# Kernel tuning notes

Hardware: AMD Instinct MI355X
Metric: run time of the kernel (lower is better)

Reference implementation:

```python
import jax, jax.numpy as jnp
import numpy as np

IN_CH, OUT_CH, K, DIL = 64, 128, 3, 8

def setup_inputs() -> dict:
    key = jax.random.key(0)
    k1, k2, k3 = jax.random.split(key, 3)
    x = jax.random.normal(k1, (16, IN_CH, 128, 128), dtype=jnp.float32)
    # xavier_normal-like init for W
    fan_in, fan_out = IN_CH * K * K, OUT_CH * K * K
    std = (2.0 / (fan_in + fan_out)) ** 0.5
    W = jax.random.normal(k2, (OUT_CH, IN_CH, K, K), dtype=jnp.float32) * std
    b = jax.random.normal(k3, (OUT_CH,), dtype=jnp.float32)
    return {"x": x, "W": W, "b": b}

def reference(x, W, b):
    pad = DIL * (K // 2)  # circular halo so output spatial size == input
    xp = jnp.pad(x, ((0, 0), (0, 0), (pad, pad), (pad, pad)), mode="wrap")
    y = jax.lax.conv_general_dilated(
        xp, W,
        window_strides=(1, 1),
        padding="VALID",
        rhs_dilation=(DIL, DIL),
        dimension_numbers=("NCHW", "OIHW", "NCHW"),
    )
    return y + b[None, :, None, None]
```

## Files before the change

kernel.cpp:

```cpp
#include <hip/hip_runtime.h>

#define IN_CH 64
#define OUT_CH 128
#define HW 128
#define KTAPS 9
#define ROWB 16384
#define ATILE 16384

typedef __bf16 bf16x8 __attribute__((ext_vector_type(8)));
typedef float f32x16 __attribute__((ext_vector_type(16)));
typedef float f32x4 __attribute__((ext_vector_type(4)));

__device__ __forceinline__ unsigned f2bf(float f) {
    unsigned u = __builtin_bit_cast(unsigned, f);
    return (u + 0x7FFFu + ((u >> 16) & 1u)) >> 16;
}

__device__ __forceinline__ int swz(int r) { return ((r ^ (r >> 3)) & 7) << 4; }

__device__ __forceinline__ void gload_lds16(const void* g, void* l) {
    __builtin_amdgcn_global_load_lds(
        (const __attribute__((address_space(1))) unsigned int*)g,
        (__attribute__((address_space(3))) unsigned int*)l, 16, 0, 0);
}

__global__ void wprep_kernel(const float* __restrict__ W, unsigned short* __restrict__ Wl) {
    int i = blockIdx.x * blockDim.x + threadIdx.x;
    if (i >= OUT_CH * IN_CH * KTAPS) return;
    int tap = i >> 13;
    int oc  = (i >> 6) & 127;
    int ic  = i & 63;
    int kh = tap / 3, kw = tap % 3;
    float v = W[((oc * IN_CH + ic) * 3 + kh) * 3 + kw];
    int addr = (oc * 128 + ic * 2) ^ swz(oc);
    *(unsigned short*)((unsigned char*)Wl + tap * ATILE + addr) = (unsigned short)f2bf(v);
}

__global__ __launch_bounds__(256, 2) void conv_kernel_f(
    const float* __restrict__ x, const unsigned short* __restrict__ Wl,
    const float* __restrict__ bias, float* __restrict__ y)
{
    __shared__ __align__(16) unsigned char xsB[3 * ROWB];
    __shared__ __align__(16) unsigned char xsA[2 * ATILE];

    int bid = blockIdx.x;
    int sb  = (bid & 7) * 256 + (bid >> 3);
    int n = sb >> 7, h = sb & 127;
    int tid = threadIdx.x;
    int wid = tid >> 6, lane = tid & 63;

    {
        const unsigned char* asrc = (const unsigned char*)Wl;
        #pragma unroll
        for (int j = 0; j < 4; ++j) {
            int off = wid * 4096 + j * 1024;
            gload_lds16(asrc + off + lane * 16, xsA + off);
        }
    }
    #pragma unroll
    for (int it = 0; it < 3; ++it) {
        int q   = it * 256 + tid;
        int w4  = q & 31;
        int ic8 = (q >> 5) & 7;
        int kh  = q >> 8;
        int srow = (h + kh * 8 + 120) & 127;
        const float* xp = x + (((n * IN_CH + ic8 * 8) * HW + srow) * HW + w4 * 4);
        f32x4 v[8];
        #pragma unroll
        for (int j = 0; j < 8; ++j)
            v[j] = *reinterpret_cast<const f32x4*>(xp + j * (HW * HW));
        #pragma unroll
        for (int j2 = 0; j2 < 4; ++j2) {
            int w = w4 * 4 + j2;
            uint4 pk;
            pk.x = f2bf(v[0][j2]) | (f2bf(v[1][j2]) << 16);
            pk.y = f2bf(v[2][j2]) | (f2bf(v[3][j2]) << 16);
            pk.z = f2bf(v[4][j2]) | (f2bf(v[5][j2]) << 16);
            pk.w = f2bf(v[6][j2]) | (f2bf(v[7][j2]) << 16);
            *reinterpret_cast<uint4*>(xsB + kh * ROWB + ((w * 128 + ic8 * 16) ^ swz(w))) = pk;
        }
    }
    __syncthreads();

    int wr = wid >> 1, wc = wid & 1;
    int l31 = lane & 31, lhi = lane >> 5;

    f32x16 acc[2][2];
    #pragma unroll
    for (int a = 0; a < 2; ++a)
        #pragma unroll
        for (int bq = 0; bq < 2; ++bq)
            #pragma unroll
            for (int r = 0; r < 16; ++r) acc[a][bq][r] = 0.0f;

    int arow0 = wr * 64 + l31, arow1 = arow0 + 32;
    int aoff0 = arow0 * 128 + lhi * 16, sa0 = swz(arow0);
    int aoff1 = arow1 * 128 + lhi * 16, sa1 = swz(arow1);

    #pragma unroll
    for (int t = 0; t < 9; ++t) {
        if (t < 8) {
            const unsigned char* asrc = (const unsigned char*)Wl + (t + 1) * ATILE;
            unsigned char* adst = xsA + ((t + 1) & 1) * ATILE;
            #pragma unroll
            for (int j = 0; j < 4; ++j) {
                int off = wid * 4096 + j * 1024;
                gload_lds16(asrc + off + lane * 16, adst + off);
            }
        }
        const unsigned char* At = xsA + (t & 1) * ATILE;
        int kh = t / 3, kw = t % 3;
        int xc0 = (wc * 64 + l31 + 8 * kw - 8) & 127;
        int xc1 = (xc0 + 32) & 127;
        int b0base = kh * ROWB + xc0 * 128 + lhi * 16, s0 = swz(xc0);
        int b1base = kh * ROWB + xc1 * 128 + lhi * 16, s1 = swz(xc1);
        #pragma unroll
        for (int ks = 0; ks < 4; ++ks) {
            bf16x8 a0 = *reinterpret_cast<const bf16x8*>(At + ((aoff0 + ks * 32) ^ sa0));
            bf16x8 a1 = *reinterpret_cast<const bf16x8*>(At + ((aoff1 + ks * 32) ^ sa1));
            bf16x8 b0 = *reinterpret_cast<const bf16x8*>(xsB + ((b0base + ks * 32) ^ s0));
            bf16x8 b1 = *reinterpret_cast<const bf16x8*>(xsB + ((b1base + ks * 32) ^ s1));
            acc[0][0] = __builtin_amdgcn_mfma_f32_32x32x16_bf16(a0, b0, acc[0][0], 0, 0, 0);
            acc[0][1] = __builtin_amdgcn_mfma_f32_32x32x16_bf16(a0, b1, acc[0][1], 0, 0, 0);
            acc[1][0] = __builtin_amdgcn_mfma_f32_32x32x16_bf16(a1, b0, acc[1][0], 0, 0, 0);
            acc[1][1] = __builtin_amdgcn_mfma_f32_32x32x16_bf16(a1, b1, acc[1][1], 0, 0, 0);
        }
        if (t < 8) __syncthreads();
    }

    int outbase = (n * OUT_CH) * HW * HW + h * HW;
    #pragma unroll
    for (int mi = 0; mi < 2; ++mi) {
        #pragma unroll
        for (int ni = 0; ni < 2; ++ni) {
            int wcol = wc * 64 + ni * 32 + l31;
            #pragma unroll
            for (int reg = 0; reg < 16; ++reg) {
                int oc = wr * 64 + mi * 32 + (reg & 3) + 8 * (reg >> 2) + 4 * lhi;
                y[outbase + oc * HW * HW + wcol] = acc[mi][ni][reg] + bias[oc];
            }
        }
    }
}

extern "C" void kernel_launch(void* const* d_in, const int* in_sizes, int n_in,
                              void* d_out, int out_size, void* d_ws, size_t ws_size,
                              hipStream_t stream) {
    const float* x = (const float*)d_in[0];
    const float* W = (const float*)d_in[1];
    const float* b = (const float*)d_in[2];
    float* y = (float*)d_out;

    unsigned short* Wl = (unsigned short*)d_ws;

    hipLaunchKernelGGL(wprep_kernel, dim3((OUT_CH * IN_CH * KTAPS + 255) / 256), dim3(256), 0, stream, W, Wl);
    hipLaunchKernelGGL(conv_kernel_f, dim3(16 * HW), dim3(256), 0, stream, x, Wl, b, y);
}
```

Baseline: 72.76 us.

## Load weight fragments directly into registers, drop LDS weight staging and barriers

The weight prep kernel now writes the bf16 weights in the exact per-lane MFMA fragment order, so each wave loads its A operands straight from global memory into a double-buffered register array. This removes the weight LDS buffer and the per-tap __syncthreads, which cuts shared memory use and allows occupancy to rise to 3 blocks per CU. The cost is higher VGPR pressure from 16 bf16x8 register buffers, plus redundant global/L2 traffic because waves in the same row group each load the same weights.

```diff
diff --git a/kernel.cpp b/kernel.cpp
--- a/kernel.cpp
+++ b/kernel.cpp
@@ -5,7 +5,6 @@
 #define HW 128
 #define KTAPS 9
 #define ROWB 16384
-#define ATILE 16384
 
 typedef __bf16 bf16x8 __attribute__((ext_vector_type(8)));
 typedef float f32x16 __attribute__((ext_vector_type(16)));
@@ -18,45 +17,43 @@
 
 __device__ __forceinline__ int swz(int r) { return ((r ^ (r >> 3)) & 7) << 4; }
 
-__device__ __forceinline__ void gload_lds16(const void* g, void* l) {
-    __builtin_amdgcn_global_load_lds(
-        (const __attribute__((address_space(1))) unsigned int*)g,
-        (__attribute__((address_space(3))) unsigned int*)l, 16, 0, 0);
-}
-
 __global__ void wprep_kernel(const float* __restrict__ W, unsigned short* __restrict__ Wl) {
     int i = blockIdx.x * blockDim.x + threadIdx.x;
     if (i >= OUT_CH * IN_CH * KTAPS) return;
-    int tap = i >> 13;
-    int oc  = (i >> 6) & 127;
-    int ic  = i & 63;
-    int kh = tap / 3, kw = tap % 3;
-    float v = W[((oc * IN_CH + ic) * 3 + kh) * 3 + kw];
-    int addr = (oc * 128 + ic * 2) ^ swz(oc);
-    *(unsigned short*)((unsigned char*)Wl + tap * ATILE + addr) = (unsigned short)f2bf(v);
+    int p  = i / 36864;
+    int r  = i % 36864;
+    int t  = r >> 12;
+    int r2 = r & 4095;
+    int m  = r2 >> 11;
+    int ks = (r2 >> 9) & 3;
+    int l  = (r2 >> 3) & 63;
+    int e  = r2 & 7;
+    int oc = p * 64 + m * 32 + (l & 31);
+    int ic = ks * 16 + (l >> 5) * 8 + e;
+    int kh = t / 3, kw = t % 3;
+    Wl[i] = (unsigned short)f2bf(W[((oc * IN_CH + ic) * 3 + kh) * 3 + kw]);
 }
 
-__global__ __launch_bounds__(256, 2) void conv_kernel_f(
+__global__ __launch_bounds__(256, 3) void conv_kernel_f(
     const float* __restrict__ x, const unsigned short* __restrict__ Wl,
     const float* __restrict__ bias, float* __restrict__ y)
 {
     __shared__ __align__(16) unsigned char xsB[3 * ROWB];
-    __shared__ __align__(16) unsigned char xsA[2 * ATILE];
 
     int bid = blockIdx.x;
     int sb  = (bid & 7) * 256 + (bid >> 3);
     int n = sb >> 7, h = sb & 127;
     int tid = threadIdx.x;
     int wid = tid >> 6, lane = tid & 63;
+    int wr = wid >> 1, wc = wid & 1;
+    int l31 = lane & 31, lhi = lane >> 5;
 
-    {
-        const unsigned char* asrc = (const unsigned char*)Wl;
-        #pragma unroll
-        for (int j = 0; j < 4; ++j) {
-            int off = wid * 4096 + j * 1024;
-            gload_lds16(asrc + off + lane * 16, xsA + off);
-        }
-    }
+    const bf16x8* Ab = reinterpret_cast<const bf16x8*>(Wl) + wr * (9 * 512) + lane;
+
+    bf16x8 aBuf[2][8];
+    #pragma unroll
+    for (int j = 0; j < 8; ++j) aBuf[0][j] = Ab[j * 64];
+
     #pragma unroll
     for (int it = 0; it < 3; ++it) {
         int q   = it * 256 + tid;
@@ -82,9 +79,6 @@
     }
     __syncthreads();
 
-    int wr = wid >> 1, wc = wid & 1;
-    int l31 = lane & 31, lhi = lane >> 5;
-
     f32x16 acc[2][2];
     #pragma unroll
     for (int a = 0; a < 2; ++a)
@@ -93,22 +87,13 @@
             #pragma unroll
             for (int r = 0; r < 16; ++r) acc[a][bq][r] = 0.0f;
 
-    int arow0 = wr * 64 + l31, arow1 = arow0 + 32;
-    int aoff0 = arow0 * 128 + lhi * 16, sa0 = swz(arow0);
-    int aoff1 = arow1 * 128 + lhi * 16, sa1 = swz(arow1);
-
     #pragma unroll
     for (int t = 0; t < 9; ++t) {
         if (t < 8) {
-            const unsigned char* asrc = (const unsigned char*)Wl + (t + 1) * ATILE;
-            unsigned char* adst = xsA + ((t + 1) & 1) * ATILE;
             #pragma unroll
-            for (int j = 0; j < 4; ++j) {
-                int off = wid * 4096 + j * 1024;
-                gload_lds16(asrc + off + lane * 16, adst + off);
-            }
+            for (int j = 0; j < 8; ++j)
+                aBuf[(t + 1) & 1][j] = Ab[(t + 1) * 512 + j * 64];
         }
-        const unsigned char* At = xsA + (t & 1) * ATILE;
         int kh = t / 3, kw = t % 3;
         int xc0 = (wc * 64 + l31 + 8 * kw - 8) & 127;
         int xc1 = (xc0 + 32) & 127;
@@ -116,8 +101,8 @@
         int b1base = kh * ROWB + xc1 * 128 + lhi * 16, s1 = swz(xc1);
         #pragma unroll
         for (int ks = 0; ks < 4; ++ks) {
-            bf16x8 a0 = *reinterpret_cast<const bf16x8*>(At + ((aoff0 + ks * 32) ^ sa0));
-            bf16x8 a1 = *reinterpret_cast<const bf16x8*>(At + ((aoff1 + ks * 32) ^ sa1));
+            bf16x8 a0 = aBuf[t & 1][ks];
+            bf16x8 a1 = aBuf[t & 1][4 + ks];
             bf16x8 b0 = *reinterpret_cast<const bf16x8*>(xsB + ((b0base + ks * 32) ^ s0));
             bf16x8 b1 = *reinterpret_cast<const bf16x8*>(xsB + ((b1base + ks * 32) ^ s1));
             acc[0][0] = __builtin_amdgcn_mfma_f32_32x32x16_bf16(a0, b0, acc[0][0], 0, 0, 0);
@@ -125,7 +110,6 @@
             acc[1][0] = __builtin_amdgcn_mfma_f32_32x32x16_bf16(a1, b0, acc[1][0], 0, 0, 0);
             acc[1][1] = __builtin_amdgcn_mfma_f32_32x32x16_bf16(a1, b1, acc[1][1], 0, 0, 0);
         }
-        if (t < 8) __syncthreads();
     }
 
     int outbase = (n * OUT_CH) * HW * HW + h * HW;
```

After: 68.25 us. 6.2% less time.
